# Optimization experiments

Measured on AMD Instinct MI355X. Metric: run time of the kernel, lower is better.

The kernel has to match this reference:

```python
import jax, jax.numpy as jnp
import numpy as np

N_NODES = 100000
N_EDGES = 1600000
N_FEAT = 64
HIDDEN = 64
N_GRAPHS = 256
BN_EPS = 1e-5


def gcn_conv(x, src, dst, edge_weight, W, b):
    # PyG GCNConv with normalize=False: linear transform, then weighted scatter-add.
    h = x @ W                                   # [N, H]
    msgs = edge_weight[:, None] * h[src]        # [E, H] gather + scale
    agg = jax.ops.segment_sum(msgs, dst, num_segments=N_NODES)  # scatter-add
    return agg + b


def setup_inputs() -> dict:
    key = jax.random.key(0)
    ks = jax.random.split(key, 12)
    x = jax.random.normal(ks[0], (N_NODES, N_FEAT), dtype=jnp.float32)
    edge_index = jax.random.randint(ks[1], (2, N_EDGES), 0, N_NODES, dtype=jnp.int64)
    edge_weight = jax.random.uniform(ks[2], (N_EDGES,), dtype=jnp.float32)
    batch = jnp.sort(jax.random.randint(ks[3], (N_NODES,), 0, N_GRAPHS, dtype=jnp.int64))
    s1 = 1.0 / np.sqrt(N_FEAT)
    s2 = 1.0 / np.sqrt(HIDDEN)
    W1 = jax.random.uniform(ks[4], (N_FEAT, HIDDEN), minval=-s1, maxval=s1)
    b1 = jnp.zeros((HIDDEN,), jnp.float32)
    W2 = jax.random.uniform(ks[5], (HIDDEN, HIDDEN), minval=-s2, maxval=s2)
    b2 = jnp.zeros((HIDDEN,), jnp.float32)
    W3 = jax.random.uniform(ks[6], (HIDDEN, HIDDEN), minval=-s2, maxval=s2)
    b3 = jnp.zeros((HIDDEN,), jnp.float32)
    gamma = jnp.ones((HIDDEN,), jnp.float32)
    beta = jnp.zeros((HIDDEN,), jnp.float32)
    linW = jax.random.uniform(ks[7], (HIDDEN, 1), minval=-s2, maxval=s2)
    linb = jnp.zeros((1,), jnp.float32)
    return {"x": x, "edge_index": edge_index, "edge_weight": edge_weight,
            "batch": batch, "W1": W1, "b1": b1, "W2": W2, "b2": b2,
            "W3": W3, "b3": b3, "gamma": gamma, "beta": beta,
            "linW": linW, "linb": linb}


def reference(x, edge_index, edge_weight, batch, W1, b1, W2, b2, W3, b3,
              gamma, beta, linW, linb):
    src, dst = edge_index[0], edge_index[1]
    h = jax.nn.relu(gcn_conv(x, src, dst, edge_weight, W1, b1))
    h = jax.nn.relu(gcn_conv(h, src, dst, edge_weight, W2, b2))
    h = gcn_conv(h, src, dst, edge_weight, W3, b3)
    # global max pool per graph -> [G, H]
    pooled = jax.ops.segment_max(h, batch, num_segments=N_GRAPHS)
    # BatchNorm1d (training mode: batch statistics, biased variance)
    mean = jnp.mean(pooled, axis=0)
    var = jnp.var(pooled, axis=0)
    normed = (pooled - mean) * jax.lax.rsqrt(var + BN_EPS) * gamma + beta
    return normed @ linW + linb  # [G, 1]
```

## Files before the change

kernel.cpp:

```cpp
#include <hip/hip_runtime.h>

#define N_NODES 100000
#define N_EDGES 1600000
#define NGRAPHS 256
#define BN_EPS 1e-5f
#define NBUK ((N_NODES + 511) >> 9)
#define BCAP 8704
#define BIN_EPB 2048
#define BIN_BLOCKS ((N_EDGES + BIN_EPB - 1) / BIN_EPB)
#define POOL_RUN 8


__device__ __forceinline__ unsigned f2ord(float f) {
  unsigned u = __float_as_uint(f);
  return (u & 0x80000000u) ? ~u : (u | 0x80000000u);
}

__device__ __forceinline__ float ord2f(unsigned u) {
  unsigned bits = (u & 0x80000000u) ? (u ^ 0x80000000u) : ~u;
  return __uint_as_float(bits);
}

__device__ __forceinline__ unsigned short f2bf(float f) {
  unsigned u = __float_as_uint(f);
  unsigned r = u + 0x7FFFu + ((u >> 16) & 1u);
  return (unsigned short)(r >> 16);
}

__device__ __forceinline__ float bf2f(unsigned short b) {
  return __uint_as_float(((unsigned)b) << 16);
}

__global__ void detect_init(const unsigned* __restrict__ ei, int* __restrict__ flag,
                            int* __restrict__ cursor) {
  const int tid = threadIdx.x;
  if (tid < NBUK) cursor[tid] = tid * BCAP;
  if (tid == 0) {
    int f = 1;
    for (int i = 1; i < 64; i += 2) {
      if (ei[i] != 0u) { f = 0; break; }
    }
    *flag = f;
  }
}

__global__ void detect_i64(const unsigned* __restrict__ ei, int* __restrict__ flag) {
  if (blockIdx.x == 0 && threadIdx.x == 0) {
    int f = 1;
    for (int i = 1; i < 64; i += 2) {
      if (ei[i] != 0u) { f = 0; break; }
    }
    *flag = f;
  }
}

__device__ __forceinline__ int load_idx(const void* p, const int* flag, long long i) {
  return (*flag) ? (int)((const long long*)p)[i] : ((const int*)p)[i];
}


__global__ __launch_bounds__(256) void binpass(const void* __restrict__ eiPtr,
                                               const int* __restrict__ flag,
                                               const float* __restrict__ ew,
                                               int* __restrict__ cursor,
                                               int2* __restrict__ tmp) {
  __shared__ int cnt[NBUK];
  __shared__ int base[NBUK];
  const int tid = threadIdx.x;
  const long long chunk0 = (long long)blockIdx.x * BIN_EPB;
  for (int i = tid; i < NBUK; i += 256) cnt[i] = 0;
  __syncthreads();
  int pk[8], wb[8], rk[8], bk[8];
  const bool i64 = (*flag != 0);
  #pragma unroll
  for (int j = 0; j < 8; ++j) {
    long long e = chunk0 + j * 256 + tid;
    rk[j] = -1;
    if (e < N_EDGES) {
      int s, d;
      if (i64) {
        const long long* ei = (const long long*)eiPtr;
        s = (int)ei[e]; d = (int)ei[N_EDGES + e];
      } else {
        const int* ei = (const int*)eiPtr;
        s = ei[e]; d = ei[N_EDGES + e];
      }
      wb[j] = __float_as_int(ew[e]);
      bk[j] = d >> 9;
      pk[j] = s | ((d & 511) << 18);
      rk[j] = atomicAdd(&cnt[bk[j]], 1);
    }
  }
  __syncthreads();
  for (int b = tid; b < NBUK; b += 256) {
    int c = cnt[b];
    base[b] = c ? atomicAdd(&cursor[b], c) : 0;
  }
  __syncthreads();
  #pragma unroll
  for (int j = 0; j < 8; ++j) {
    if (rk[j] >= 0) {
      int pos = base[bk[j]] + rk[j];
      if (pos < (bk[j] + 1) * BCAP) {
        int2 r; r.x = pk[j]; r.y = wb[j];
        tmp[pos] = r;
      }
    }
  }
}

__global__ __launch_bounds__(256) void place2(const int2* __restrict__ tmp,
                                              const int* __restrict__ cursor,
                                              int2* __restrict__ rowPtr2,
                                              int2* __restrict__ csrP) {
  __shared__ int cnt[512];
  __shared__ int sc[256];
  __shared__ int cur[512];
  const int b = blockIdx.x;
  const int tid = threadIdx.x;
  const int beg = b * BCAP;
  int cntb = cursor[b] - beg;
  if (cntb > BCAP) cntb = BCAP;
  const int end = beg + cntb;
  cnt[tid] = 0; cnt[tid + 256] = 0;
  __syncthreads();
  for (int i = beg + tid; i < end; i += 256) {
    atomicAdd(&cnt[(tmp[i].x >> 18) & 511], 1);
  }
  __syncthreads();
  int c0 = cnt[2 * tid], c1 = cnt[2 * tid + 1];
  int pairSum = c0 + c1;
  sc[tid] = pairSum;
  __syncthreads();
  for (int off = 1; off < 256; off <<= 1) {
    int t = (tid >= off) ? sc[tid - off] : 0;
    __syncthreads();
    sc[tid] += t;
    __syncthreads();
  }
  int exclPair = sc[tid] - pairSum;
  int base0 = beg + exclPair;
  int base1 = base0 + c0;
  int g0 = (b << 9) + 2 * tid;
  if (g0 < N_NODES)     { int2 r; r.x = base0; r.y = base0 + c0; rowPtr2[g0] = r; }
  if (g0 + 1 < N_NODES) { int2 r; r.x = base1; r.y = base1 + c1; rowPtr2[g0 + 1] = r; }
  cur[2 * tid] = base0;
  cur[2 * tid + 1] = base1;
  __syncthreads();
  for (int i = beg + tid; i < end; i += 256) {
    int2 e = tmp[i];
    int pos = atomicAdd(&cur[(e.x >> 18) & 511], 1);
    int2 r; r.x = e.x & 0x3FFFF; r.y = e.y;
    csrP[pos] = r;
  }
}


template<bool F32IN>
__global__ __launch_bounds__(256) void gemm_u(const void* __restrict__ Ain,
                                              const float* __restrict__ W,
                                              unsigned short* __restrict__ Uout,
                                              int N) {
  __shared__ float Wt[64][68];
  __shared__ float At[64][68];
  const int tid = threadIdx.x;
  const int rowBase = blockIdx.x * 64;

  for (int i = tid; i < 4096; i += 256) {
    int k = i >> 6, c = i & 63;
    Wt[c][k] = W[i];
  }
  if (F32IN) {
    const float4* A4 = (const float4*)Ain;
    #pragma unroll
    for (int j = 0; j < 4; ++j) {
      int t4 = tid + j * 256;
      int g4 = rowBase * 16 + t4;
      float4 v = make_float4(0.f, 0.f, 0.f, 0.f);
      if (g4 < N * 16) v = A4[g4];
      int r = t4 >> 4, k4 = t4 & 15;
      *(float4*)&At[r][k4 * 4] = v;
    }
  } else {
    const uint4* A16 = (const uint4*)Ain;
    #pragma unroll
    for (int j = 0; j < 2; ++j) {
      int q = tid + j * 256;
      int r = q >> 3, c8 = (q & 7) * 8;
      int grow = rowBase + r;
      uint4 v = make_uint4(0u, 0u, 0u, 0u);
      if (grow < N) v = A16[(size_t)grow * 8 + (q & 7)];
      float4 f0, f1;
      f0.x = bf2f((unsigned short)(v.x & 0xFFFFu)); f0.y = bf2f((unsigned short)(v.x >> 16));
      f0.z = bf2f((unsigned short)(v.y & 0xFFFFu)); f0.w = bf2f((unsigned short)(v.y >> 16));
      f1.x = bf2f((unsigned short)(v.z & 0xFFFFu)); f1.y = bf2f((unsigned short)(v.z >> 16));
      f1.z = bf2f((unsigned short)(v.w & 0xFFFFu)); f1.w = bf2f((unsigned short)(v.w >> 16));
      *(float4*)&At[r][c8] = f0;
      *(float4*)&At[r][c8 + 4] = f1;
    }
  }
  __syncthreads();

  const int c = tid & 63;
  const int r0 = (tid >> 6) * 16;
  float acc[16];
  #pragma unroll
  for (int i = 0; i < 16; ++i) acc[i] = 0.f;

  for (int k0 = 0; k0 < 64; k0 += 4) {
    float4 w = *(const float4*)&Wt[c][k0];
    #pragma unroll
    for (int i = 0; i < 16; ++i) {
      float4 a = *(const float4*)&At[r0 + i][k0];
      acc[i] += a.x * w.x + a.y * w.y + a.z * w.z + a.w * w.w;
    }
  }

  #pragma unroll
  for (int i = 0; i < 16; ++i) {
    int row = rowBase + r0 + i;
    if (row < N) Uout[(size_t)row * 64 + c] = f2bf(acc[i]);
  }
}


__device__ __forceinline__ float gather_node_scalar(const unsigned short* __restrict__ T,
                                                    const int2* __restrict__ csr,
                                                    int beg, int end, int lane) {
  float a0 = 0.f, a1 = 0.f, a2 = 0.f, a3 = 0.f;
  int i = beg;
  for (; i + 16 <= end; i += 16) {
    int2 m[16];
    #pragma unroll
    for (int j = 0; j < 16; ++j) m[j] = csr[i + j];
    float v[16];
    #pragma unroll
    for (int j = 0; j < 16; ++j) v[j] = bf2f(T[(size_t)m[j].x * 64 + lane]);
    #pragma unroll
    for (int j = 0; j < 16; j += 4) {
      a0 = fmaf(__int_as_float(m[j].y),     v[j],     a0);
      a1 = fmaf(__int_as_float(m[j + 1].y), v[j + 1], a1);
      a2 = fmaf(__int_as_float(m[j + 2].y), v[j + 2], a2);
      a3 = fmaf(__int_as_float(m[j + 3].y), v[j + 3], a3);
    }
  }
  while (i < end) {
    const int last = end - 1;
    int2 m[8]; float w[8];
    #pragma unroll
    for (int j = 0; j < 8; ++j) {
      int idx = i + j;
      int c = idx < last ? idx : last;
      m[j] = csr[c];
      w[j] = (idx < end) ? __int_as_float(m[j].y) : 0.f;
    }
    float v[8];
    #pragma unroll
    for (int j = 0; j < 8; ++j) v[j] = bf2f(T[(size_t)m[j].x * 64 + lane]);
    #pragma unroll
    for (int j = 0; j < 8; j += 4) {
      a0 = fmaf(w[j],     v[j],     a0);
      a1 = fmaf(w[j + 1], v[j + 1], a1);
      a2 = fmaf(w[j + 2], v[j + 2], a2);
      a3 = fmaf(w[j + 3], v[j + 3], a3);
    }
    i += 8;
  }
  return (a0 + a1) + (a2 + a3);
}


__global__ __launch_bounds__(256) void pull_relu(const unsigned short* __restrict__ T,
                                                 const int2* __restrict__ rowPtr2,
                                                 const int2* __restrict__ csr,
                                                 const float* __restrict__ bias,
                                                 unsigned short* __restrict__ Hout) {
  int wid = __builtin_amdgcn_readfirstlane((blockIdx.x * 256 + threadIdx.x) >> 6);
  const int lane = threadIdx.x & 63;
  if (wid >= N_NODES) return;
  const int2 be = rowPtr2[wid];
  float acc = gather_node_scalar(T, csr, be.x, be.y, lane);
  float v = fmaxf(acc + bias[lane], 0.f);
  Hout[(size_t)wid * 64 + lane] = f2bf(v);
}


__global__ __launch_bounds__(256) void pull_pool(const unsigned short* __restrict__ T,
                                                 const int2* __restrict__ rowPtr2,
                                                 const int2* __restrict__ csr,
                                                 const float* __restrict__ bias,
                                                 const void* __restrict__ bPtr,
                                                 const int* __restrict__ flag,
                                                 unsigned* __restrict__ pooled) {
  int wseq = __builtin_amdgcn_readfirstlane((blockIdx.x * 256 + threadIdx.x) >> 6);
  const int lane = threadIdx.x & 63;
  const int n0 = wseq * POOL_RUN;
  if (n0 >= N_NODES) return;
  const int n1 = min(n0 + POOL_RUN, N_NODES);
  const float blane = bias[lane];
  int curg = load_idx(bPtr, flag, n0);
  float best = -3.4e38f;
  for (int n = n0; n < n1; ++n) {
    const int2 be = rowPtr2[n];
    float acc = gather_node_scalar(T, csr, be.x, be.y, lane);
    float v = acc + blane;
    int g = load_idx(bPtr, flag, n);
    if (g != curg) {
      atomicMax(&pooled[curg * 64 + lane], f2ord(best));
      curg = g; best = v;
    } else {
      best = fmaxf(best, v);
    }
  }
  atomicMax(&pooled[curg * 64 + lane], f2ord(best));
}


template<bool RELU_IN, bool ADD_BIAS, bool RELU_OUT>
__global__ __launch_bounds__(256) void gemm64(const float* A,
                                              const float* __restrict__ W,
                                              const float* __restrict__ b,
                                              float* C, int N) {
  __shared__ float Wt[64][68];
  __shared__ float At[64][68];
  const int tid = threadIdx.x;
  const int rowBase = blockIdx.x * 64;

  for (int i = tid; i < 4096; i += 256) {
    int k = i >> 6, c = i & 63;
    Wt[c][k] = W[i];
  }
  const float4* A4 = (const float4*)A;
  #pragma unroll
  for (int j = 0; j < 4; ++j) {
    int t4 = tid + j * 256;
    int g4 = rowBase * 16 + t4;
    float4 v = make_float4(0.f, 0.f, 0.f, 0.f);
    if (g4 < N * 16) v = A4[g4];
    if (RELU_IN) {
      v.x = fmaxf(v.x, 0.f); v.y = fmaxf(v.y, 0.f);
      v.z = fmaxf(v.z, 0.f); v.w = fmaxf(v.w, 0.f);
    }
    int r = t4 >> 4, k4 = t4 & 15;
    *(float4*)&At[r][k4 * 4] = v;
  }
  __syncthreads();

  const int c = tid & 63;
  const int r0 = (tid >> 6) * 16;
  float acc[16];
  #pragma unroll
  for (int i = 0; i < 16; ++i) acc[i] = 0.f;

  for (int k0 = 0; k0 < 64; k0 += 4) {
    float4 w = *(const float4*)&Wt[c][k0];
    #pragma unroll
    for (int i = 0; i < 16; ++i) {
      float4 a = *(const float4*)&At[r0 + i][k0];
      acc[i] += a.x * w.x + a.y * w.y + a.z * w.z + a.w * w.w;
    }
  }

  const float bias = ADD_BIAS ? b[c] : 0.f;
  #pragma unroll
  for (int i = 0; i < 16; ++i) {
    int row = rowBase + r0 + i;
    if (row < N) {
      float v = acc[i] + bias;
      if (RELU_OUT) v = fmaxf(v, 0.f);
      C[row * 64 + c] = v;
    }
  }
}

__global__ __launch_bounds__(256) void init_bias(float* __restrict__ agg,
                                                 const float* __restrict__ b, int n4) {
  int i = blockIdx.x * 256 + threadIdx.x;
  if (i >= n4) return;
  ((float4*)agg)[i] = ((const float4*)b)[i & 15];
}

__global__ __launch_bounds__(256) void scatter_add(const float* __restrict__ h,
                                                   const void* __restrict__ eiPtr,
                                                   const int* __restrict__ flag,
                                                   const float* __restrict__ ew,
                                                   float* __restrict__ agg) {
  int gtid = blockIdx.x * 256 + threadIdx.x;
  int e = gtid >> 6, lane = gtid & 63;
  if (e >= N_EDGES) return;
  int s = load_idx(eiPtr, flag, e);
  int d = load_idx(eiPtr, flag, (long long)N_EDGES + e);
  atomicAdd(&agg[d * 64 + lane], ew[e] * h[s * 64 + lane]);
}

__global__ __launch_bounds__(256) void seg_max(const float* __restrict__ h,
                                               const void* __restrict__ bPtr,
                                               const int* __restrict__ flag,
                                               unsigned* __restrict__ pooled) {
  int gtid = blockIdx.x * 256 + threadIdx.x;
  int n = gtid >> 6, lane = gtid & 63;
  if (n >= N_NODES) return;
  int g = load_idx(bPtr, flag, n);
  atomicMax(&pooled[g * 64 + lane], f2ord(h[n * 64 + lane]));
}


__global__ __launch_bounds__(256) void bn_head(const unsigned* __restrict__ pooled,
                                               const float* __restrict__ gamma,
                                               const float* __restrict__ beta,
                                               const float* __restrict__ linW,
                                               const float* __restrict__ linb,
                                               float* __restrict__ out) {
  __shared__ float P[NGRAPHS][64 + 1];
  __shared__ float mean_s[64], rstd_s[64];
  const int tid = threadIdx.x;

  for (int i = tid; i < NGRAPHS * 64; i += 256) {
    P[i >> 6][i & 63] = ord2f(pooled[i]);
  }
  __syncthreads();

  if (tid < 64) {
    float s = 0.f, ss = 0.f;
    for (int g = 0; g < NGRAPHS; ++g) {
      float v = P[g][tid];
      s += v; ss += v * v;
    }
    float m = s / (float)NGRAPHS;
    float var = ss / (float)NGRAPHS - m * m;
    mean_s[tid] = m;
    rstd_s[tid] = rsqrtf(var + BN_EPS);
  }
  __syncthreads();

  float acc = linb[0];
  #pragma unroll 8
  for (int c = 0; c < 64; ++c) {
    float normed = (P[tid][c] - mean_s[c]) * rstd_s[c] * gamma[c] + beta[c];
    acc += normed * linW[c];
  }
  out[tid] = acc;
}


extern "C" void kernel_launch(void* const* d_in, const int* in_sizes, int n_in,
                              void* d_out, int out_size, void* d_ws, size_t ws_size,
                              hipStream_t stream) {
  const float* x     = (const float*)d_in[0];
  const void*  ei    = d_in[1];
  const float* ew    = (const float*)d_in[2];
  const void*  batch = d_in[3];
  const float* W1    = (const float*)d_in[4];
  const float* b1    = (const float*)d_in[5];
  const float* W2    = (const float*)d_in[6];
  const float* b2    = (const float*)d_in[7];
  const float* W3    = (const float*)d_in[8];
  const float* b3    = (const float*)d_in[9];
  const float* gamma = (const float*)d_in[10];
  const float* beta  = (const float*)d_in[11];
  const float* linW  = (const float*)d_in[12];
  const float* linb  = (const float*)d_in[13];

  char* ws = (char*)d_ws;
  const size_t MAT  = (size_t)N_NODES * 64 * sizeof(float);
  const size_t TBL  = (size_t)N_NODES * 64 * sizeof(unsigned short);
  const size_t CSRP = (size_t)NBUK * BCAP * sizeof(int2);
  const size_t PTR2 = ((size_t)N_NODES * sizeof(int2) + 255) & ~(size_t)255;

  size_t off = 0;
  unsigned short* uA = (unsigned short*)(ws + off); off += TBL;
  unsigned short* hB = (unsigned short*)(ws + off); off += TBL;
  int2*  csrP   = (int2*)(ws + off);           off += CSRP;
  int2*  rowPtr2 = (int2*)(ws + off);          off += PTR2;
  int*   cursor = (int*)(ws + off);            off += 1024;
  unsigned* pooled = (unsigned*)(ws + off);    off += (size_t)NGRAPHS * 64 * sizeof(unsigned);
  int*   flag   = (int*)(ws + off);            off += 256;
  const bool csrPath = (ws_size >= off);

  const int gemmBlocks = (N_NODES + 63) / 64;
  const int nodeWaveBlocks = (N_NODES * 64) / 256;
  const int poolBlocks = (N_NODES + POOL_RUN * 4 - 1) / (POOL_RUN * 4);

  if (csrPath) {
    int2* tmpP = (int2*)uA;
    detect_init<<<1, 256, 0, stream>>>((const unsigned*)ei, flag, cursor);
    binpass<<<BIN_BLOCKS, 256, 0, stream>>>(ei, flag, ew, cursor, tmpP);
    place2<<<NBUK, 256, 0, stream>>>(tmpP, cursor, rowPtr2, csrP);

    gemm_u<true><<<gemmBlocks, 256, 0, stream>>>(x, W1, uA, N_NODES);
    pull_relu<<<nodeWaveBlocks, 256, 0, stream>>>(uA, rowPtr2, csrP, b1, hB);
    gemm_u<false><<<gemmBlocks, 256, 0, stream>>>(hB, W2, uA, N_NODES);
    pull_relu<<<nodeWaveBlocks, 256, 0, stream>>>(uA, rowPtr2, csrP, b2, hB);
    gemm_u<false><<<gemmBlocks, 256, 0, stream>>>(hB, W3, uA, N_NODES);
    hipMemsetAsync(pooled, 0, (size_t)NGRAPHS * 64 * sizeof(unsigned), stream);
    pull_pool<<<poolBlocks, 256, 0, stream>>>(uA, rowPtr2, csrP, b3, batch, flag, pooled);

    bn_head<<<1, 256, 0, stream>>>(pooled, gamma, beta, linW, linb, (float*)d_out);
  } else {
    float* h   = (float*)ws;
    float* agg = (float*)(ws + MAT);
    unsigned* pooled2 = (unsigned*)(ws + 2 * MAT);
    int* flag2 = (int*)(ws + 2 * MAT + (size_t)NGRAPHS * 64 * sizeof(unsigned));
    detect_i64<<<1, 64, 0, stream>>>((const unsigned*)ei, flag2);
    const int n4 = N_NODES * 16;
    const int initBlocks = (n4 + 255) / 256;
    const int scatBlocks = (N_EDGES * 64) / 256;

    gemm64<false, false, false><<<gemmBlocks, 256, 0, stream>>>(x, W1, b1, h, N_NODES);
    init_bias<<<initBlocks, 256, 0, stream>>>(agg, b1, n4);
    scatter_add<<<scatBlocks, 256, 0, stream>>>(h, ei, flag2, ew, agg);
    gemm64<true, false, false><<<gemmBlocks, 256, 0, stream>>>(agg, W2, b2, h, N_NODES);
    init_bias<<<initBlocks, 256, 0, stream>>>(agg, b2, n4);
    scatter_add<<<scatBlocks, 256, 0, stream>>>(h, ei, flag2, ew, agg);
    gemm64<true, false, false><<<gemmBlocks, 256, 0, stream>>>(agg, W3, b3, h, N_NODES);
    init_bias<<<initBlocks, 256, 0, stream>>>(agg, b3, n4);
    scatter_add<<<scatBlocks, 256, 0, stream>>>(h, ei, flag2, ew, agg);

    hipMemsetAsync(pooled2, 0, (size_t)NGRAPHS * 64 * sizeof(unsigned), stream);
    seg_max<<<nodeWaveBlocks, 256, 0, stream>>>(agg, batch, flag2, pooled2);
    bn_head<<<1, 256, 0, stream>>>(pooled2, gamma, beta, linW, linb, (float*)d_out);
  }
}
```

Measured before the change: 281.5 us.

## Fuse CSR placement with first GEMM and software-pipeline the edge gather

Merges the CSR placement kernel and the first feature GEMM into one launch by splitting blocks by index. This needs a separate tmp buffer, since uA is now written concurrently. The pooled-buffer memset moves into the init kernel. The per-node gather loop becomes a double-buffered 8-edge pipeline that issues the next batch's loads before doing the FMAs of the current one, aiming to hide gather latency. The trade-offs are extra workspace, higher register pressure in the gather, and dropping the 16-wide unrolled loop.

```diff
diff --git a/kernel.cpp b/kernel.cpp
--- a/kernel.cpp
+++ b/kernel.cpp
@@ -32,9 +32,10 @@
 }
 
 __global__ void detect_init(const unsigned* __restrict__ ei, int* __restrict__ flag,
-                            int* __restrict__ cursor) {
+                            int* __restrict__ cursor, unsigned* __restrict__ pooled) {
   const int tid = threadIdx.x;
   if (tid < NBUK) cursor[tid] = tid * BCAP;
+  for (int i = tid; i < NGRAPHS * 64; i += 256) pooled[i] = 0u;
   if (tid == 0) {
     int f = 1;
     for (int i = 1; i < 64; i += 2) {
@@ -109,55 +110,98 @@
   }
 }
 
-__global__ __launch_bounds__(256) void place2(const int2* __restrict__ tmp,
-                                              const int* __restrict__ cursor,
-                                              int2* __restrict__ rowPtr2,
-                                              int2* __restrict__ csrP) {
-  __shared__ int cnt[512];
-  __shared__ int sc[256];
-  __shared__ int cur[512];
-  const int b = blockIdx.x;
+
+__global__ __launch_bounds__(256) void place2_gemm1(
+    const int2* __restrict__ tmp, const int* __restrict__ cursor,
+    int2* __restrict__ rowPtr2, int2* __restrict__ csrP,
+    const float* __restrict__ x, const float* __restrict__ W,
+    unsigned short* __restrict__ Uout) {
+  __shared__ float smem[2][64][68];
   const int tid = threadIdx.x;
-  const int beg = b * BCAP;
-  int cntb = cursor[b] - beg;
-  if (cntb > BCAP) cntb = BCAP;
-  const int end = beg + cntb;
-  cnt[tid] = 0; cnt[tid + 256] = 0;
-  __syncthreads();
-  for (int i = beg + tid; i < end; i += 256) {
-    atomicAdd(&cnt[(tmp[i].x >> 18) & 511], 1);
-  }
-  __syncthreads();
-  int c0 = cnt[2 * tid], c1 = cnt[2 * tid + 1];
-  int pairSum = c0 + c1;
-  sc[tid] = pairSum;
-  __syncthreads();
-  for (int off = 1; off < 256; off <<= 1) {
-    int t = (tid >= off) ? sc[tid - off] : 0;
+
+  if (blockIdx.x < NBUK) {
+    int* cnt = (int*)&smem[0][0][0];
+    int* sc  = cnt + 512;
+    int* cur = sc + 256;
+    const int b = blockIdx.x;
+    const int beg = b * BCAP;
+    int cntb = cursor[b] - beg;
+    if (cntb > BCAP) cntb = BCAP;
+    const int end = beg + cntb;
+    cnt[tid] = 0; cnt[tid + 256] = 0;
     __syncthreads();
-    sc[tid] += t;
+    for (int i = beg + tid; i < end; i += 256) {
+      atomicAdd(&cnt[(tmp[i].x >> 18) & 511], 1);
+    }
     __syncthreads();
-  }
-  int exclPair = sc[tid] - pairSum;
-  int base0 = beg + exclPair;
-  int base1 = base0 + c0;
-  int g0 = (b << 9) + 2 * tid;
-  if (g0 < N_NODES)     { int2 r; r.x = base0; r.y = base0 + c0; rowPtr2[g0] = r; }
-  if (g0 + 1 < N_NODES) { int2 r; r.x = base1; r.y = base1 + c1; rowPtr2[g0 + 1] = r; }
-  cur[2 * tid] = base0;
-  cur[2 * tid + 1] = base1;
-  __syncthreads();
-  for (int i = beg + tid; i < end; i += 256) {
-    int2 e = tmp[i];
-    int pos = atomicAdd(&cur[(e.x >> 18) & 511], 1);
-    int2 r; r.x = e.x & 0x3FFFF; r.y = e.y;
-    csrP[pos] = r;
-  }
-}
-
-
-template<bool F32IN>
-__global__ __launch_bounds__(256) void gemm_u(const void* __restrict__ Ain,
+    int c0 = cnt[2 * tid], c1 = cnt[2 * tid + 1];
+    int pairSum = c0 + c1;
+    sc[tid] = pairSum;
+    __syncthreads();
+    for (int off = 1; off < 256; off <<= 1) {
+      int t = (tid >= off) ? sc[tid - off] : 0;
+      __syncthreads();
+      sc[tid] += t;
+      __syncthreads();
+    }
+    int exclPair = sc[tid] - pairSum;
+    int base0 = beg + exclPair;
+    int base1 = base0 + c0;
+    int g0 = (b << 9) + 2 * tid;
+    if (g0 < N_NODES)     { int2 r; r.x = base0; r.y = base0 + c0; rowPtr2[g0] = r; }
+    if (g0 + 1 < N_NODES) { int2 r; r.x = base1; r.y = base1 + c1; rowPtr2[g0 + 1] = r; }
+    cur[2 * tid] = base0;
+    cur[2 * tid + 1] = base1;
+    __syncthreads();
+    for (int i = beg + tid; i < end; i += 256) {
+      int2 e = tmp[i];
+      int pos = atomicAdd(&cur[(e.x >> 18) & 511], 1);
+      int2 r; r.x = e.x & 0x3FFFF; r.y = e.y;
+      csrP[pos] = r;
+    }
+  } else {
+    const int rowBase = (blockIdx.x - NBUK) * 64;
+    float (*Wt)[68] = (float(*)[68])&smem[0][0][0];
+    float (*At)[68] = (float(*)[68])&smem[1][0][0];
+    for (int i = tid; i < 4096; i += 256) {
+      int k = i >> 6, c = i & 63;
+      Wt[c][k] = W[i];
+    }
+    const float4* A4 = (const float4*)x;
+    #pragma unroll
+    for (int j = 0; j < 4; ++j) {
+      int t4 = tid + j * 256;
+      int g4 = rowBase * 16 + t4;
+      float4 v = make_float4(0.f, 0.f, 0.f, 0.f);
+      if (g4 < N_NODES * 16) v = A4[g4];
+      int r = t4 >> 4, k4 = t4 & 15;
+      *(float4*)&At[r][k4 * 4] = v;
+    }
+    __syncthreads();
+
+    const int c = tid & 63;
+    const int r0 = (tid >> 6) * 16;
+    float acc[16];
+    #pragma unroll
+    for (int i = 0; i < 16; ++i) acc[i] = 0.f;
+    for (int k0 = 0; k0 < 64; k0 += 4) {
+      float4 w = *(const float4*)&Wt[c][k0];
+      #pragma unroll
+      for (int i = 0; i < 16; ++i) {
+        float4 a = *(const float4*)&At[r0 + i][k0];
+        acc[i] += a.x * w.x + a.y * w.y + a.z * w.z + a.w * w.w;
+      }
+    }
+    #pragma unroll
+    for (int i = 0; i < 16; ++i) {
+      int row = rowBase + r0 + i;
+      if (row < N_NODES) Uout[(size_t)row * 64 + c] = f2bf(acc[i]);
+    }
+  }
+}
+
+
+__global__ __launch_bounds__(256) void gemm_u(const unsigned short* __restrict__ Ain,
                                               const float* __restrict__ W,
                                               unsigned short* __restrict__ Uout,
                                               int N) {
@@ -170,34 +214,21 @@
     int k = i >> 6, c = i & 63;
     Wt[c][k] = W[i];
   }
-  if (F32IN) {
-    const float4* A4 = (const float4*)Ain;
-    #pragma unroll
-    for (int j = 0; j < 4; ++j) {
-      int t4 = tid + j * 256;
-      int g4 = rowBase * 16 + t4;
-      float4 v = make_float4(0.f, 0.f, 0.f, 0.f);
-      if (g4 < N * 16) v = A4[g4];
-      int r = t4 >> 4, k4 = t4 & 15;
-      *(float4*)&At[r][k4 * 4] = v;
-    }
-  } else {
-    const uint4* A16 = (const uint4*)Ain;
-    #pragma unroll
-    for (int j = 0; j < 2; ++j) {
-      int q = tid + j * 256;
-      int r = q >> 3, c8 = (q & 7) * 8;
-      int grow = rowBase + r;
-      uint4 v = make_uint4(0u, 0u, 0u, 0u);
-      if (grow < N) v = A16[(size_t)grow * 8 + (q & 7)];
-      float4 f0, f1;
-      f0.x = bf2f((unsigned short)(v.x & 0xFFFFu)); f0.y = bf2f((unsigned short)(v.x >> 16));
-      f0.z = bf2f((unsigned short)(v.y & 0xFFFFu)); f0.w = bf2f((unsigned short)(v.y >> 16));
-      f1.x = bf2f((unsigned short)(v.z & 0xFFFFu)); f1.y = bf2f((unsigned short)(v.z >> 16));
-      f1.z = bf2f((unsigned short)(v.w & 0xFFFFu)); f1.w = bf2f((unsigned short)(v.w >> 16));
-      *(float4*)&At[r][c8] = f0;
-      *(float4*)&At[r][c8 + 4] = f1;
-    }
+  const uint4* A16 = (const uint4*)Ain;
+  #pragma unroll
+  for (int j = 0; j < 2; ++j) {
+    int q = tid + j * 256;
+    int r = q >> 3, c8 = (q & 7) * 8;
+    int grow = rowBase + r;
+    uint4 v = make_uint4(0u, 0u, 0u, 0u);
+    if (grow < N) v = A16[(size_t)grow * 8 + (q & 7)];
+    float4 f0, f1;
+    f0.x = bf2f((unsigned short)(v.x & 0xFFFFu)); f0.y = bf2f((unsigned short)(v.x >> 16));
+    f0.z = bf2f((unsigned short)(v.y & 0xFFFFu)); f0.w = bf2f((unsigned short)(v.y >> 16));
+    f1.x = bf2f((unsigned short)(v.z & 0xFFFFu)); f1.y = bf2f((unsigned short)(v.z >> 16));
+    f1.z = bf2f((unsigned short)(v.w & 0xFFFFu)); f1.w = bf2f((unsigned short)(v.w >> 16));
+    *(float4*)&At[r][c8] = f0;
+    *(float4*)&At[r][c8 + 4] = f1;
   }
   __syncthreads();
 
@@ -224,47 +255,59 @@
 }
 
 
-__device__ __forceinline__ float gather_node_scalar(const unsigned short* __restrict__ T,
-                                                    const int2* __restrict__ csr,
-                                                    int beg, int end, int lane) {
+struct GBatch { int2 m[8]; float w[8]; float v[8]; };
+
+__device__ __forceinline__ void gload(GBatch& B, const int2* __restrict__ csr,
+                                      int i, int end,
+                                      const unsigned short* __restrict__ T, int lane) {
+  const int last = end - 1;
+  #pragma unroll
+  for (int j = 0; j < 8; ++j) {
+    int idx = i + j;
+    int c = idx < last ? idx : last;
+    B.m[j] = csr[c];
+    B.w[j] = (idx < end) ? __int_as_float(B.m[j].y) : 0.f;
+  }
+  #pragma unroll
+  for (int j = 0; j < 8; ++j)
+    B.v[j] = bf2f(T[(size_t)B.m[j].x * 64 + lane]);
+}
+
+__device__ __forceinline__ void gfma(const GBatch& B, float& a0, float& a1,
+                                     float& a2, float& a3) {
+  a0 = fmaf(B.w[0], B.v[0], a0);
+  a1 = fmaf(B.w[1], B.v[1], a1);
+  a2 = fmaf(B.w[2], B.v[2], a2);
+  a3 = fmaf(B.w[3], B.v[3], a3);
+  a0 = fmaf(B.w[4], B.v[4], a0);
+  a1 = fmaf(B.w[5], B.v[5], a1);
+  a2 = fmaf(B.w[6], B.v[6], a2);
+  a3 = fmaf(B.w[7], B.v[7], a3);
+}
+
+__device__ __forceinline__ float gather_pipe(const unsigned short* __restrict__ T,
+                                             const int2* __restrict__ csr,
+                                             int beg, int end, int lane) {
+  const int cnt = end - beg;
+  if (cnt <= 0) return 0.f;
   float a0 = 0.f, a1 = 0.f, a2 = 0.f, a3 = 0.f;
-  int i = beg;
-  for (; i + 16 <= end; i += 16) {
-    int2 m[16];
-    #pragma unroll
-    for (int j = 0; j < 16; ++j) m[j] = csr[i + j];
-    float v[16];
-    #pragma unroll
-    for (int j = 0; j < 16; ++j) v[j] = bf2f(T[(size_t)m[j].x * 64 + lane]);
-    #pragma unroll
-    for (int j = 0; j < 16; j += 4) {
-      a0 = fmaf(__int_as_float(m[j].y),     v[j],     a0);
-      a1 = fmaf(__int_as_float(m[j + 1].y), v[j + 1], a1);
-      a2 = fmaf(__int_as_float(m[j + 2].y), v[j + 2], a2);
-      a3 = fmaf(__int_as_float(m[j + 3].y), v[j + 3], a3);
-    }
-  }
-  while (i < end) {
-    const int last = end - 1;
-    int2 m[8]; float w[8];
-    #pragma unroll
-    for (int j = 0; j < 8; ++j) {
-      int idx = i + j;
-      int c = idx < last ? idx : last;
-      m[j] = csr[c];
-      w[j] = (idx < end) ? __int_as_float(m[j].y) : 0.f;
-    }
-    float v[8];
-    #pragma unroll
-    for (int j = 0; j < 8; ++j) v[j] = bf2f(T[(size_t)m[j].x * 64 + lane]);
-    #pragma unroll
-    for (int j = 0; j < 8; j += 4) {
-      a0 = fmaf(w[j],     v[j],     a0);
-      a1 = fmaf(w[j + 1], v[j + 1], a1);
-      a2 = fmaf(w[j + 2], v[j + 2], a2);
-      a3 = fmaf(w[j + 3], v[j + 3], a3);
-    }
-    i += 8;
+  GBatch A, B;
+  const int nb = (cnt + 7) >> 3;
+  gload(A, csr, beg, end, T, lane);
+  int b = 1;
+  while (b + 1 < nb) {
+    gload(B, csr, beg + 8 * b, end, T, lane);
+    gfma(A, a0, a1, a2, a3);
+    gload(A, csr, beg + 8 * (b + 1), end, T, lane);
+    gfma(B, a0, a1, a2, a3);
+    b += 2;
+  }
+  if (b < nb) {
+    gload(B, csr, beg + 8 * b, end, T, lane);
+    gfma(A, a0, a1, a2, a3);
+    gfma(B, a0, a1, a2, a3);
+  } else {
+    gfma(A, a0, a1, a2, a3);
   }
   return (a0 + a1) + (a2 + a3);
 }
@@ -279,9 +322,8 @@
   const int lane = threadIdx.x & 63;
   if (wid >= N_NODES) return;
   const int2 be = rowPtr2[wid];
-  float acc = gather_node_scalar(T, csr, be.x, be.y, lane);
-  float v = fmaxf(acc + bias[lane], 0.f);
-  Hout[(size_t)wid * 64 + lane] = f2bf(v);
+  float acc = gather_pipe(T, csr, be.x, be.y, lane);
+  Hout[(size_t)wid * 64 + lane] = f2bf(fmaxf(acc + bias[lane], 0.f));
 }
 
 
@@ -302,7 +344,7 @@
   float best = -3.4e38f;
   for (int n = n0; n < n1; ++n) {
     const int2 be = rowPtr2[n];
-    float acc = gather_node_scalar(T, csr, be.x, be.y, lane);
+    float acc = gather_pipe(T, csr, be.x, be.y, lane);
     float v = acc + blane;
     int g = load_idx(bPtr, flag, n);
     if (g != curg) {
@@ -471,6 +513,7 @@
   unsigned short* uA = (unsigned short*)(ws + off); off += TBL;
   unsigned short* hB = (unsigned short*)(ws + off); off += TBL;
   int2*  csrP   = (int2*)(ws + off);           off += CSRP;
+  int2*  tmpP   = (int2*)(ws + off);           off += CSRP;
   int2*  rowPtr2 = (int2*)(ws + off);          off += PTR2;
   int*   cursor = (int*)(ws + off);            off += 1024;
   unsigned* pooled = (unsigned*)(ws + off);    off += (size_t)NGRAPHS * 64 * sizeof(unsigned);
@@ -482,17 +525,15 @@
   const int poolBlocks = (N_NODES + POOL_RUN * 4 - 1) / (POOL_RUN * 4);
 
   if (csrPath) {
-    int2* tmpP = (int2*)uA;
-    detect_init<<<1, 256, 0, stream>>>((const unsigned*)ei, flag, cursor);
+    detect_init<<<1, 256, 0, stream>>>((const unsigned*)ei, flag, cursor, pooled);
     binpass<<<BIN_BLOCKS, 256, 0, stream>>>(ei, flag, ew, cursor, tmpP);
-    place2<<<NBUK, 256, 0, stream>>>(tmpP, cursor, rowPtr2, csrP);
-
-    gemm_u<true><<<gemmBlocks, 256, 0, stream>>>(x, W1, uA, N_NODES);
+    place2_gemm1<<<NBUK + gemmBlocks, 256, 0, stream>>>(tmpP, cursor, rowPtr2, csrP,
+                                                        x, W1, uA);
+
     pull_relu<<<nodeWaveBlocks, 256, 0, stream>>>(uA, rowPtr2, csrP, b1, hB);
-    gemm_u<false><<<gemmBlocks, 256, 0, stream>>>(hB, W2, uA, N_NODES);
+    gemm_u<<<gemmBlocks, 256, 0, stream>>>(hB, W2, uA, N_NODES);
     pull_relu<<<nodeWaveBlocks, 256, 0, stream>>>(uA, rowPtr2, csrP, b2, hB);
-    gemm_u<false><<<gemmBlocks, 256, 0, stream>>>(hB, W3, uA, N_NODES);
-    hipMemsetAsync(pooled, 0, (size_t)NGRAPHS * 64 * sizeof(unsigned), stream);
+    gemm_u<<<gemmBlocks, 256, 0, stream>>>(hB, W3, uA, N_NODES);
     pull_pool<<<poolBlocks, 256, 0, stream>>>(uA, rowPtr2, csrP, b3, batch, flag, pooled);
 
     bn_head<<<1, 256, 0, stream>>>(pooled, gamma, beta, linW, linb, (float*)d_out);
```

Result: slower. 290.4 us (+3.2%).
